# Optimization experiments

Measured on AMD Instinct MI355X. Metric: run time of the kernel, lower is better.

## Reference

```python
import jax, jax.numpy as jnp
import numpy as np
from jax import lax

IN_FEATURES = 8192
OUT_FEATURES = 28672


def _unpack3(qweight, infeatures):
    """Unpack GPTQ-style 3-bit weights.

    qweight: (infeatures//32*3, O) int32. Every 3 consecutive int32 rows hold
    32 packed 3-bit values per column (GPTQ quant.py packing): values 0-9 in
    word0 bits [0..30), value 10 split over word0[30:32]|word1[0:1],
    values 11-20 in word1 bits [1..31), value 21 split over word1[31:32]|word2[0:2],
    values 22-31 in word2 bits [2..32).
    Returns float32 (infeatures, O) with raw quant codes in [0, 8).
    """
    O = qweight.shape[1]
    G = infeatures // 32
    q = lax.bitcast_convert_type(qweight, jnp.uint32).reshape(G, 3, O)
    w0, w1, w2 = q[:, 0], q[:, 1], q[:, 2]
    sh = jnp.arange(10, dtype=jnp.uint32)  # 10 whole values per word
    v0 = (w0[:, None, :] >> (3 * sh)[None, :, None]) & 7          # (G,10,O)
    v10 = (((w0 >> 30) & 3) | ((w1 & 1) << 2))[:, None, :]        # (G,1,O)
    v1 = (w1[:, None, :] >> (3 * sh + 1)[None, :, None]) & 7       # (G,10,O)
    v21 = (((w1 >> 31) & 1) | ((w2 & 3) << 1))[:, None, :]        # (G,1,O)
    v2 = (w2[:, None, :] >> (3 * sh + 2)[None, :, None]) & 7       # (G,10,O)
    vals = jnp.concatenate([v0, v10, v1, v21, v2], axis=1)        # (G,32,O)
    return vals.reshape(infeatures, O).astype(jnp.float32)


def setup_inputs() -> dict:
    key = jax.random.key(0)
    k1, k2, k3, k4, k5 = jax.random.split(key, 5)
    x = jax.random.normal(k1, (1, IN_FEATURES), dtype=jnp.float32)
    qweight = jax.random.randint(k2, (IN_FEATURES // 32 * 3, OUT_FEATURES), 0, 2147483647, dtype=jnp.int32)
    scales = jax.random.uniform(k3, (OUT_FEATURES, 1), dtype=jnp.float32)
    zeros = jax.random.normal(k4, (OUT_FEATURES, 1), dtype=jnp.float32)
    bias = jax.random.normal(k5, (OUT_FEATURES,), dtype=jnp.float32)
    return {"x": x, "qweight": qweight, "scales": scales, "zeros": zeros, "bias": bias}


def reference(x, qweight, scales, zeros, bias):
    infeatures = x.shape[-1]
    q = _unpack3(qweight, infeatures)            # (K, O) float codes
    # per-output-channel dequant: W[k, o] = scales[o] * q[k, o] - zeros[o]
    W = scales.T * q - zeros.T                   # (K, O)
    y = x @ W + bias                             # (1, O)
    return y
```

## Files before the change

kernel.cpp:

```cpp
#include <hip/hip_runtime.h>
#include <stdint.h>


constexpr int O_FEAT  = 28672;
constexpr int IN_FEAT = 8192;
constexpr int NGROUP  = IN_FEAT / 32;
constexpr int SPLIT   = 32;
constexpr int GPB     = NGROUP / SPLIT;
constexpr int O4      = O_FEAT / 4;
constexpr int NBX     = O4 / 64;
constexpr int PFD     = 4;

template <int SH>
__device__ __forceinline__ void q3e4(uint32_t va, uint32_t vb, uint32_t vc, uint32_t vd,
                                     uint32_t m7, float xj,
                                     float& A, float& B, float& C, float& D) {
  float t0, t1, t2, t3;
  if constexpr (SH < 20) {
    asm("v_lshlrev_b32 %0, %12, %8\n\t"
        "v_lshlrev_b32 %1, %12, %9\n\t"
        "v_lshlrev_b32 %2, %12, %10\n\t"
        "v_lshlrev_b32 %3, %12, %11\n\t"
        "v_and_or_b32 %0, %0, %13, 2.0\n\t"
        "v_and_or_b32 %1, %1, %13, 2.0\n\t"
        "v_and_or_b32 %2, %2, %13, 2.0\n\t"
        "v_and_or_b32 %3, %3, %13, 2.0\n\t"
        "v_fmac_f32 %4, %14, %0\n\t"
        "v_fmac_f32 %5, %14, %1\n\t"
        "v_fmac_f32 %6, %14, %2\n\t"
        "v_fmac_f32 %7, %14, %3"
        : "=&v"(t0), "=&v"(t1), "=&v"(t2), "=&v"(t3),
          "+v"(A), "+v"(B), "+v"(C), "+v"(D)
        : "v"(va), "v"(vb), "v"(vc), "v"(vd), "n"(20 - SH), "s"(m7), "v"(xj));
  } else if constexpr (SH == 20) {
    asm("v_and_or_b32 %0, %8, %12, 2.0\n\t"
        "v_and_or_b32 %1, %9, %12, 2.0\n\t"
        "v_and_or_b32 %2, %10, %12, 2.0\n\t"
        "v_and_or_b32 %3, %11, %12, 2.0\n\t"
        "v_fmac_f32 %4, %13, %0\n\t"
        "v_fmac_f32 %5, %13, %1\n\t"
        "v_fmac_f32 %6, %13, %2\n\t"
        "v_fmac_f32 %7, %13, %3"
        : "=&v"(t0), "=&v"(t1), "=&v"(t2), "=&v"(t3),
          "+v"(A), "+v"(B), "+v"(C), "+v"(D)
        : "v"(va), "v"(vb), "v"(vc), "v"(vd), "s"(m7), "v"(xj));
  } else {
    asm("v_lshrrev_b32 %0, %12, %8\n\t"
        "v_lshrrev_b32 %1, %12, %9\n\t"
        "v_lshrrev_b32 %2, %12, %10\n\t"
        "v_lshrrev_b32 %3, %12, %11\n\t"
        "v_and_or_b32 %0, %0, %13, 2.0\n\t"
        "v_and_or_b32 %1, %1, %13, 2.0\n\t"
        "v_and_or_b32 %2, %2, %13, 2.0\n\t"
        "v_and_or_b32 %3, %3, %13, 2.0\n\t"
        "v_fmac_f32 %4, %14, %0\n\t"
        "v_fmac_f32 %5, %14, %1\n\t"
        "v_fmac_f32 %6, %14, %2\n\t"
        "v_fmac_f32 %7, %14, %3"
        : "=&v"(t0), "=&v"(t1), "=&v"(t2), "=&v"(t3),
          "+v"(A), "+v"(B), "+v"(C), "+v"(D)
        : "v"(va), "v"(vb), "v"(vc), "v"(vd), "n"(SH - 20), "s"(m7), "v"(xj));
  }
}

__device__ __forceinline__ void q3e4_s10(uint4 wa, uint4 wb, uint32_t m3, uint32_t m4,
                                         float xj, float& A, float& B, float& C, float& D) {
  float t0, t1, t2, t3, u0, u1, u2, u3;
  asm("v_lshrrev_b32 %0, 10, %12\n\t"
      "v_lshrrev_b32 %1, 10, %13\n\t"
      "v_lshrrev_b32 %2, 10, %14\n\t"
      "v_lshrrev_b32 %3, 10, %15\n\t"
      "v_lshlrev_b32 %4, 22, %16\n\t"
      "v_lshlrev_b32 %5, 22, %17\n\t"
      "v_lshlrev_b32 %6, 22, %18\n\t"
      "v_lshlrev_b32 %7, 22, %19\n\t"
      "v_and_or_b32 %0, %0, %20, 2.0\n\t"
      "v_and_or_b32 %1, %1, %20, 2.0\n\t"
      "v_and_or_b32 %2, %2, %20, 2.0\n\t"
      "v_and_or_b32 %3, %3, %20, 2.0\n\t"
      "v_and_or_b32 %0, %4, %21, %0\n\t"
      "v_and_or_b32 %1, %5, %21, %1\n\t"
      "v_and_or_b32 %2, %6, %21, %2\n\t"
      "v_and_or_b32 %3, %7, %21, %3\n\t"
      "v_fmac_f32 %8, %22, %0\n\t"
      "v_fmac_f32 %9, %22, %1\n\t"
      "v_fmac_f32 %10, %22, %2\n\t"
      "v_fmac_f32 %11, %22, %3"
      : "=&v"(t0), "=&v"(t1), "=&v"(t2), "=&v"(t3),
        "=&v"(u0), "=&v"(u1), "=&v"(u2), "=&v"(u3),
        "+v"(A), "+v"(B), "+v"(C), "+v"(D)
      : "v"(wa.x), "v"(wa.y), "v"(wa.z), "v"(wa.w),
        "v"(wb.x), "v"(wb.y), "v"(wb.z), "v"(wb.w),
        "s"(m3), "s"(m4), "v"(xj));
}

__device__ __forceinline__ void q3e4_s21(uint4 wb, uint4 wc, uint32_t m1, uint32_t m6,
                                         float xj, float& A, float& B, float& C, float& D) {
  float t0, t1, t2, t3, u0, u1, u2, u3;
  asm("v_lshrrev_b32 %0, 11, %12\n\t"
      "v_lshrrev_b32 %1, 11, %13\n\t"
      "v_lshrrev_b32 %2, 11, %14\n\t"
      "v_lshrrev_b32 %3, 11, %15\n\t"
      "v_lshlrev_b32 %4, 21, %16\n\t"
      "v_lshlrev_b32 %5, 21, %17\n\t"
      "v_lshlrev_b32 %6, 21, %18\n\t"
      "v_lshlrev_b32 %7, 21, %19\n\t"
      "v_and_or_b32 %0, %0, %20, 2.0\n\t"
      "v_and_or_b32 %1, %1, %20, 2.0\n\t"
      "v_and_or_b32 %2, %2, %20, 2.0\n\t"
      "v_and_or_b32 %3, %3, %20, 2.0\n\t"
      "v_and_or_b32 %0, %4, %21, %0\n\t"
      "v_and_or_b32 %1, %5, %21, %1\n\t"
      "v_and_or_b32 %2, %6, %21, %2\n\t"
      "v_and_or_b32 %3, %7, %21, %3\n\t"
      "v_fmac_f32 %8, %22, %0\n\t"
      "v_fmac_f32 %9, %22, %1\n\t"
      "v_fmac_f32 %10, %22, %2\n\t"
      "v_fmac_f32 %11, %22, %3"
      : "=&v"(t0), "=&v"(t1), "=&v"(t2), "=&v"(t3),
        "=&v"(u0), "=&v"(u1), "=&v"(u2), "=&v"(u3),
        "+v"(A), "+v"(B), "+v"(C), "+v"(D)
      : "v"(wb.x), "v"(wb.y), "v"(wb.z), "v"(wb.w),
        "v"(wc.x), "v"(wc.y), "v"(wc.z), "v"(wc.w),
        "s"(m1), "s"(m6), "v"(xj));
}

__global__ __launch_bounds__(64) void q3_onepass(const float* __restrict__ x,
                                                 const uint4* __restrict__ qw4,
                                                 const float* __restrict__ scales,
                                                 const float* __restrict__ zeros,
                                                 const float* __restrict__ bias,
                                                 float* __restrict__ out) {
  const int tcol4 = blockIdx.x * 64 + threadIdx.x;
  const int g0    = blockIdx.y * GPB;
  const uint4* qp = qw4 + (size_t)(3 * g0) * O4 + tcol4;

  __shared__ float xs[GPB * 32];
  const float4 xt = reinterpret_cast<const float4*>(x + g0 * 32)[threadIdx.x];
  reinterpret_cast<float4*>(xs)[threadIdx.x] = xt;

  const uint32_t m7 = 0x00700000u, m3 = 0x00300000u, m4 = 0x00400000u,
                 m1 = 0x00100000u, m6 = 0x00600000u;

  float A = 0.f, B = 0.f, C = 0.f, D = 0.f;

  uint4 w[GPB][3];
  #pragma unroll
  for (int g = 0; g < PFD; ++g) {
    w[g][0] = qp[0]; w[g][1] = qp[O4]; w[g][2] = qp[2 * O4];
    qp += 3 * O4;
  }

  #pragma unroll
  for (int g = 0; g < GPB; ++g) {
    if (g + PFD < GPB) {
      w[g + PFD][0] = qp[0]; w[g + PFD][1] = qp[O4]; w[g + PFD][2] = qp[2 * O4];
      qp += 3 * O4;
    }
    const uint4 wa = w[g][0], wb = w[g][1], wc = w[g][2];

    float xv[32];
    const float4* s4 = reinterpret_cast<const float4*>(&xs[g * 32]);
    #pragma unroll
    for (int u = 0; u < 8; ++u) {
      float4 t = s4[u];
      xv[4 * u + 0] = t.x; xv[4 * u + 1] = t.y;
      xv[4 * u + 2] = t.z; xv[4 * u + 3] = t.w;
    }

    q3e4<0>(wa.x, wa.y, wa.z, wa.w, m7, xv[0], A, B, C, D);
    q3e4<3>(wa.x, wa.y, wa.z, wa.w, m7, xv[1], A, B, C, D);
    q3e4<6>(wa.x, wa.y, wa.z, wa.w, m7, xv[2], A, B, C, D);
    q3e4<9>(wa.x, wa.y, wa.z, wa.w, m7, xv[3], A, B, C, D);
    q3e4<12>(wa.x, wa.y, wa.z, wa.w, m7, xv[4], A, B, C, D);
    q3e4<15>(wa.x, wa.y, wa.z, wa.w, m7, xv[5], A, B, C, D);
    q3e4<18>(wa.x, wa.y, wa.z, wa.w, m7, xv[6], A, B, C, D);
    q3e4<21>(wa.x, wa.y, wa.z, wa.w, m7, xv[7], A, B, C, D);
    q3e4<24>(wa.x, wa.y, wa.z, wa.w, m7, xv[8], A, B, C, D);
    q3e4<27>(wa.x, wa.y, wa.z, wa.w, m7, xv[9], A, B, C, D);
    q3e4_s10(wa, wb, m3, m4, xv[10], A, B, C, D);
    q3e4<1>(wb.x, wb.y, wb.z, wb.w, m7, xv[11], A, B, C, D);
    q3e4<4>(wb.x, wb.y, wb.z, wb.w, m7, xv[12], A, B, C, D);
    q3e4<7>(wb.x, wb.y, wb.z, wb.w, m7, xv[13], A, B, C, D);
    q3e4<10>(wb.x, wb.y, wb.z, wb.w, m7, xv[14], A, B, C, D);
    q3e4<13>(wb.x, wb.y, wb.z, wb.w, m7, xv[15], A, B, C, D);
    q3e4<16>(wb.x, wb.y, wb.z, wb.w, m7, xv[16], A, B, C, D);
    q3e4<19>(wb.x, wb.y, wb.z, wb.w, m7, xv[17], A, B, C, D);
    q3e4<22>(wb.x, wb.y, wb.z, wb.w, m7, xv[18], A, B, C, D);
    q3e4<25>(wb.x, wb.y, wb.z, wb.w, m7, xv[19], A, B, C, D);
    q3e4<28>(wb.x, wb.y, wb.z, wb.w, m7, xv[20], A, B, C, D);
    q3e4_s21(wb, wc, m1, m6, xv[21], A, B, C, D);
    q3e4<2>(wc.x, wc.y, wc.z, wc.w, m7, xv[22], A, B, C, D);
    q3e4<5>(wc.x, wc.y, wc.z, wc.w, m7, xv[23], A, B, C, D);
    q3e4<8>(wc.x, wc.y, wc.z, wc.w, m7, xv[24], A, B, C, D);
    q3e4<11>(wc.x, wc.y, wc.z, wc.w, m7, xv[25], A, B, C, D);
    q3e4<14>(wc.x, wc.y, wc.z, wc.w, m7, xv[26], A, B, C, D);
    q3e4<17>(wc.x, wc.y, wc.z, wc.w, m7, xv[27], A, B, C, D);
    q3e4<20>(wc.x, wc.y, wc.z, wc.w, m7, xv[28], A, B, C, D);
    q3e4<23>(wc.x, wc.y, wc.z, wc.w, m7, xv[29], A, B, C, D);
    q3e4<26>(wc.x, wc.y, wc.z, wc.w, m7, xv[30], A, B, C, D);
    q3e4<29>(wc.x, wc.y, wc.z, wc.w, m7, xv[31], A, B, C, D);
  }

  const float4 sc = reinterpret_cast<const float4*>(scales)[tcol4];
  float4 contrib;
  contrib.x = 4.f * sc.x * A;
  contrib.y = 4.f * sc.y * B;
  contrib.z = 4.f * sc.z * C;
  contrib.w = 4.f * sc.w * D;

  if (blockIdx.y == 0) {
    float s = 0.f;
    const float4* xall = reinterpret_cast<const float4*>(x);
    #pragma unroll
    for (int i = 0; i < (IN_FEAT / 4) / 64; ++i) {
      float4 t = xall[i * 64 + threadIdx.x];
      s += (t.x + t.y) + (t.z + t.w);
    }
    #pragma unroll
    for (int off = 32; off > 0; off >>= 1) s += __shfl_xor(s, off, 64);
    const float S = s;
    const float4 zr = reinterpret_cast<const float4*>(zeros)[tcol4];
    const float4 bi = reinterpret_cast<const float4*>(bias)[tcol4];
    contrib.x += bi.x - (8.f * sc.x + zr.x) * S;
    contrib.y += bi.y - (8.f * sc.y + zr.y) * S;
    contrib.z += bi.z - (8.f * sc.z + zr.z) * S;
    contrib.w += bi.w - (8.f * sc.w + zr.w) * S;
  }

  float* op = out + 4 * (size_t)tcol4;
  atomicAdd(op + 0, contrib.x);
  atomicAdd(op + 1, contrib.y);
  atomicAdd(op + 2, contrib.z);
  atomicAdd(op + 3, contrib.w);
}

extern "C" void kernel_launch(void* const* d_in, const int* in_sizes, int n_in,
                              void* d_out, int out_size, void* d_ws, size_t ws_size,
                              hipStream_t stream) {
  const float* x      = (const float*)d_in[0];
  const uint4* qw4    = (const uint4*)d_in[1];
  const float* scales = (const float*)d_in[2];
  const float* zeros  = (const float*)d_in[3];
  const float* bias   = (const float*)d_in[4];
  float*       out    = (float*)d_out;

  q3_onepass<<<dim3(NBX, SPLIT), dim3(64), 0, stream>>>(x, qw4, scales, zeros,
                                                        bias, out);
}
```

Before: 138.9 us.

## Load activations via scalar loads into SGPRs, double-buffered, instead of LDS

The activation slice is no longer staged through shared memory and read into VGPRs. Each 32-element group is instead fetched with s_load_dwordx16 into SGPRs, with the next group prefetched while the current one is consumed, and the FMAs take x as a scalar operand. This drops the LDS store/load traffic and frees VGPRs. Weight prefetch depth is cut from 4 to 2 groups, which may expose more global load latency. The lgkmcnt(0) wait at the end of each group may also stall on scalar memory latency.

```diff
diff --git a/kernel.cpp b/kernel.cpp
--- a/kernel.cpp
+++ b/kernel.cpp
@@ -9,7 +9,20 @@
 constexpr int GPB     = NGROUP / SPLIT;
 constexpr int O4      = O_FEAT / 4;
 constexpr int NBX     = O4 / 64;
-constexpr int PFD     = 4;
+constexpr int PFD     = 2;
+
+typedef float sf16 __attribute__((ext_vector_type(16)));
+
+__device__ __forceinline__ void sload_x(const float* p, sf16& lo, sf16& hi) {
+  asm volatile("s_load_dwordx16 %0, %2, 0\n\t"
+               "s_load_dwordx16 %1, %2, 64"
+               : "=s"(lo), "=s"(hi)
+               : "s"(p));
+}
+
+__device__ __forceinline__ void swait(sf16& lo, sf16& hi) {
+  asm volatile("s_waitcnt lgkmcnt(0)" : "+s"(lo), "+s"(hi));
+}
 
 template <int SH>
 __device__ __forceinline__ void q3e4(uint32_t va, uint32_t vb, uint32_t vc, uint32_t vd,
@@ -31,7 +44,7 @@
         "v_fmac_f32 %7, %14, %3"
         : "=&v"(t0), "=&v"(t1), "=&v"(t2), "=&v"(t3),
           "+v"(A), "+v"(B), "+v"(C), "+v"(D)
-        : "v"(va), "v"(vb), "v"(vc), "v"(vd), "n"(20 - SH), "s"(m7), "v"(xj));
+        : "v"(va), "v"(vb), "v"(vc), "v"(vd), "n"(20 - SH), "s"(m7), "s"(xj));
   } else if constexpr (SH == 20) {
     asm("v_and_or_b32 %0, %8, %12, 2.0\n\t"
         "v_and_or_b32 %1, %9, %12, 2.0\n\t"
@@ -43,7 +56,7 @@
         "v_fmac_f32 %7, %13, %3"
         : "=&v"(t0), "=&v"(t1), "=&v"(t2), "=&v"(t3),
           "+v"(A), "+v"(B), "+v"(C), "+v"(D)
-        : "v"(va), "v"(vb), "v"(vc), "v"(vd), "s"(m7), "v"(xj));
+        : "v"(va), "v"(vb), "v"(vc), "v"(vd), "s"(m7), "s"(xj));
   } else {
     asm("v_lshrrev_b32 %0, %12, %8\n\t"
         "v_lshrrev_b32 %1, %12, %9\n\t"
@@ -59,7 +72,7 @@
         "v_fmac_f32 %7, %14, %3"
         : "=&v"(t0), "=&v"(t1), "=&v"(t2), "=&v"(t3),
           "+v"(A), "+v"(B), "+v"(C), "+v"(D)
-        : "v"(va), "v"(vb), "v"(vc), "v"(vd), "n"(SH - 20), "s"(m7), "v"(xj));
+        : "v"(va), "v"(vb), "v"(vc), "v"(vd), "n"(SH - 20), "s"(m7), "s"(xj));
   }
 }
 
@@ -91,7 +104,7 @@
         "+v"(A), "+v"(B), "+v"(C), "+v"(D)
       : "v"(wa.x), "v"(wa.y), "v"(wa.z), "v"(wa.w),
         "v"(wb.x), "v"(wb.y), "v"(wb.z), "v"(wb.w),
-        "s"(m3), "s"(m4), "v"(xj));
+        "s"(m3), "s"(m4), "s"(xj));
 }
 
 __device__ __forceinline__ void q3e4_s21(uint4 wb, uint4 wc, uint32_t m1, uint32_t m6,
@@ -122,7 +135,7 @@
         "+v"(A), "+v"(B), "+v"(C), "+v"(D)
       : "v"(wb.x), "v"(wb.y), "v"(wb.z), "v"(wb.w),
         "v"(wc.x), "v"(wc.y), "v"(wc.z), "v"(wc.w),
-        "s"(m1), "s"(m6), "v"(xj));
+        "s"(m1), "s"(m6), "s"(xj));
 }
 
 __global__ __launch_bounds__(64) void q3_onepass(const float* __restrict__ x,
@@ -134,15 +147,16 @@
   const int tcol4 = blockIdx.x * 64 + threadIdx.x;
   const int g0    = blockIdx.y * GPB;
   const uint4* qp = qw4 + (size_t)(3 * g0) * O4 + tcol4;
-
-  __shared__ float xs[GPB * 32];
-  const float4 xt = reinterpret_cast<const float4*>(x + g0 * 32)[threadIdx.x];
-  reinterpret_cast<float4*>(xs)[threadIdx.x] = xt;
+  const float* xb = x + g0 * 32;
 
   const uint32_t m7 = 0x00700000u, m3 = 0x00300000u, m4 = 0x00400000u,
                  m1 = 0x00100000u, m6 = 0x00600000u;
 
   float A = 0.f, B = 0.f, C = 0.f, D = 0.f;
+
+  sf16 xa0, xa1, xb0, xb1;
+  sload_x(xb, xa0, xa1);
+  swait(xa0, xa1);
 
   uint4 w[GPB][3];
   #pragma unroll
@@ -153,53 +167,54 @@
 
   #pragma unroll
   for (int g = 0; g < GPB; ++g) {
+    const bool odd = (g & 1);
+    sf16& clo = odd ? xb0 : xa0;
+    sf16& chi = odd ? xb1 : xa1;
+    sf16& nlo = odd ? xa0 : xb0;
+    sf16& nhi = odd ? xa1 : xb1;
+
+    if (g + 1 < GPB) sload_x(xb + (g + 1) * 32, nlo, nhi);
+
     if (g + PFD < GPB) {
       w[g + PFD][0] = qp[0]; w[g + PFD][1] = qp[O4]; w[g + PFD][2] = qp[2 * O4];
       qp += 3 * O4;
     }
     const uint4 wa = w[g][0], wb = w[g][1], wc = w[g][2];
 
-    float xv[32];
-    const float4* s4 = reinterpret_cast<const float4*>(&xs[g * 32]);
-    #pragma unroll
-    for (int u = 0; u < 8; ++u) {
-      float4 t = s4[u];
-      xv[4 * u + 0] = t.x; xv[4 * u + 1] = t.y;
-      xv[4 * u + 2] = t.z; xv[4 * u + 3] = t.w;
-    }
-
-    q3e4<0>(wa.x, wa.y, wa.z, wa.w, m7, xv[0], A, B, C, D);
-    q3e4<3>(wa.x, wa.y, wa.z, wa.w, m7, xv[1], A, B, C, D);
-    q3e4<6>(wa.x, wa.y, wa.z, wa.w, m7, xv[2], A, B, C, D);
-    q3e4<9>(wa.x, wa.y, wa.z, wa.w, m7, xv[3], A, B, C, D);
-    q3e4<12>(wa.x, wa.y, wa.z, wa.w, m7, xv[4], A, B, C, D);
-    q3e4<15>(wa.x, wa.y, wa.z, wa.w, m7, xv[5], A, B, C, D);
-    q3e4<18>(wa.x, wa.y, wa.z, wa.w, m7, xv[6], A, B, C, D);
-    q3e4<21>(wa.x, wa.y, wa.z, wa.w, m7, xv[7], A, B, C, D);
-    q3e4<24>(wa.x, wa.y, wa.z, wa.w, m7, xv[8], A, B, C, D);
-    q3e4<27>(wa.x, wa.y, wa.z, wa.w, m7, xv[9], A, B, C, D);
-    q3e4_s10(wa, wb, m3, m4, xv[10], A, B, C, D);
-    q3e4<1>(wb.x, wb.y, wb.z, wb.w, m7, xv[11], A, B, C, D);
-    q3e4<4>(wb.x, wb.y, wb.z, wb.w, m7, xv[12], A, B, C, D);
-    q3e4<7>(wb.x, wb.y, wb.z, wb.w, m7, xv[13], A, B, C, D);
-    q3e4<10>(wb.x, wb.y, wb.z, wb.w, m7, xv[14], A, B, C, D);
-    q3e4<13>(wb.x, wb.y, wb.z, wb.w, m7, xv[15], A, B, C, D);
-    q3e4<16>(wb.x, wb.y, wb.z, wb.w, m7, xv[16], A, B, C, D);
-    q3e4<19>(wb.x, wb.y, wb.z, wb.w, m7, xv[17], A, B, C, D);
-    q3e4<22>(wb.x, wb.y, wb.z, wb.w, m7, xv[18], A, B, C, D);
-    q3e4<25>(wb.x, wb.y, wb.z, wb.w, m7, xv[19], A, B, C, D);
-    q3e4<28>(wb.x, wb.y, wb.z, wb.w, m7, xv[20], A, B, C, D);
-    q3e4_s21(wb, wc, m1, m6, xv[21], A, B, C, D);
-    q3e4<2>(wc.x, wc.y, wc.z, wc.w, m7, xv[22], A, B, C, D);
-    q3e4<5>(wc.x, wc.y, wc.z, wc.w, m7, xv[23], A, B, C, D);
-    q3e4<8>(wc.x, wc.y, wc.z, wc.w, m7, xv[24], A, B, C, D);
-    q3e4<11>(wc.x, wc.y, wc.z, wc.w, m7, xv[25], A, B, C, D);
-    q3e4<14>(wc.x, wc.y, wc.z, wc.w, m7, xv[26], A, B, C, D);
-    q3e4<17>(wc.x, wc.y, wc.z, wc.w, m7, xv[27], A, B, C, D);
-    q3e4<20>(wc.x, wc.y, wc.z, wc.w, m7, xv[28], A, B, C, D);
-    q3e4<23>(wc.x, wc.y, wc.z, wc.w, m7, xv[29], A, B, C, D);
-    q3e4<26>(wc.x, wc.y, wc.z, wc.w, m7, xv[30], A, B, C, D);
-    q3e4<29>(wc.x, wc.y, wc.z, wc.w, m7, xv[31], A, B, C, D);
+    q3e4<0>(wa.x, wa.y, wa.z, wa.w, m7, clo[0], A, B, C, D);
+    q3e4<3>(wa.x, wa.y, wa.z, wa.w, m7, clo[1], A, B, C, D);
+    q3e4<6>(wa.x, wa.y, wa.z, wa.w, m7, clo[2], A, B, C, D);
+    q3e4<9>(wa.x, wa.y, wa.z, wa.w, m7, clo[3], A, B, C, D);
+    q3e4<12>(wa.x, wa.y, wa.z, wa.w, m7, clo[4], A, B, C, D);
+    q3e4<15>(wa.x, wa.y, wa.z, wa.w, m7, clo[5], A, B, C, D);
+    q3e4<18>(wa.x, wa.y, wa.z, wa.w, m7, clo[6], A, B, C, D);
+    q3e4<21>(wa.x, wa.y, wa.z, wa.w, m7, clo[7], A, B, C, D);
+    q3e4<24>(wa.x, wa.y, wa.z, wa.w, m7, clo[8], A, B, C, D);
+    q3e4<27>(wa.x, wa.y, wa.z, wa.w, m7, clo[9], A, B, C, D);
+    q3e4_s10(wa, wb, m3, m4, clo[10], A, B, C, D);
+    q3e4<1>(wb.x, wb.y, wb.z, wb.w, m7, clo[11], A, B, C, D);
+    q3e4<4>(wb.x, wb.y, wb.z, wb.w, m7, clo[12], A, B, C, D);
+    q3e4<7>(wb.x, wb.y, wb.z, wb.w, m7, clo[13], A, B, C, D);
+    q3e4<10>(wb.x, wb.y, wb.z, wb.w, m7, clo[14], A, B, C, D);
+    q3e4<13>(wb.x, wb.y, wb.z, wb.w, m7, clo[15], A, B, C, D);
+    q3e4<16>(wb.x, wb.y, wb.z, wb.w, m7, chi[0], A, B, C, D);
+    q3e4<19>(wb.x, wb.y, wb.z, wb.w, m7, chi[1], A, B, C, D);
+    q3e4<22>(wb.x, wb.y, wb.z, wb.w, m7, chi[2], A, B, C, D);
+    q3e4<25>(wb.x, wb.y, wb.z, wb.w, m7, chi[3], A, B, C, D);
+    q3e4<28>(wb.x, wb.y, wb.z, wb.w, m7, chi[4], A, B, C, D);
+    q3e4_s21(wb, wc, m1, m6, chi[5], A, B, C, D);
+    q3e4<2>(wc.x, wc.y, wc.z, wc.w, m7, chi[6], A, B, C, D);
+    q3e4<5>(wc.x, wc.y, wc.z, wc.w, m7, chi[7], A, B, C, D);
+    q3e4<8>(wc.x, wc.y, wc.z, wc.w, m7, chi[8], A, B, C, D);
+    q3e4<11>(wc.x, wc.y, wc.z, wc.w, m7, chi[9], A, B, C, D);
+    q3e4<14>(wc.x, wc.y, wc.z, wc.w, m7, chi[10], A, B, C, D);
+    q3e4<17>(wc.x, wc.y, wc.z, wc.w, m7, chi[11], A, B, C, D);
+    q3e4<20>(wc.x, wc.y, wc.z, wc.w, m7, chi[12], A, B, C, D);
+    q3e4<23>(wc.x, wc.y, wc.z, wc.w, m7, chi[13], A, B, C, D);
+    q3e4<26>(wc.x, wc.y, wc.z, wc.w, m7, chi[14], A, B, C, D);
+    q3e4<29>(wc.x, wc.y, wc.z, wc.w, m7, chi[15], A, B, C, D);
+
+    if (g + 1 < GPB) swait(nlo, nhi);
   }
 
   const float4 sc = reinterpret_cast<const float4*>(scales)[tcol4];
```

Result: no change. 139.1 us (+0.2%).
